# Kernel optimization log

Hardware: AMD Instinct MI355X
Metric: run time of the kernel (lower is better)

The kernel has to match this reference:

```python
import jax, jax.numpy as jnp
import numpy as np

FIXED_FRAMES = 30
# MediaPipe Holistic landmark layout: 468 face, 21 left hand, 33 pose, 21 right hand = 543
LIPS = np.array([61, 185, 40, 39, 37, 0, 267, 269, 270, 409, 291,
                 146, 91, 181, 84, 17, 314, 405, 321, 375,
                 78, 191, 80, 81, 82, 13, 312, 311, 310, 415,
                 95, 88, 178, 87, 14, 317, 402, 318, 324, 308], dtype=np.int32)
LEFT_HAND = np.arange(468, 489, dtype=np.int32)          # 21
UPPER_BODY = np.arange(489, 489 + 25, dtype=np.int32)    # 25 upper-body pose landmarks
RIGHT_HAND = np.arange(522, 543, dtype=np.int32)         # 21
SEL = np.concatenate([LIPS, LEFT_HAND, UPPER_BODY, RIGHT_HAND])  # 107 landmarks

N_FRAMES = 16384
N_LANDMARKS = 543

def setup_inputs() -> dict:
    key = jax.random.key(0)
    k1, k2 = jax.random.split(key)
    x = jax.random.normal(k1, (N_FRAMES, N_LANDMARKS, 3), dtype=jnp.float32)
    nan_mask = jax.random.uniform(k2, x.shape) < 0.1
    x = jnp.where(nan_mask, jnp.nan, x)
    return {"x_in": x}

def _normalize_gather(x_in):
    # Global nan-aware mean over ALL elements (scalar), as x[~isnan(x)].mean()
    mask = ~jnp.isnan(x_in)
    cnt = jnp.sum(mask).astype(x_in.dtype)
    xs = jnp.where(mask, x_in, 0.0)
    mean = jnp.sum(xs) / cnt
    xc = jnp.where(mask, x_in - mean, 0.0)
    # torch.std of the centered non-NaN values (unbiased, re-subtracts its own mean)
    m2 = jnp.sum(xc) / cnt
    var = jnp.sum(jnp.where(mask, (xc - m2) ** 2, 0.0)) / (cnt - 1.0)
    std = jnp.sqrt(var)
    y = jnp.where(mask, xc / std, 0.0)  # normalize; NaN positions -> 0 (x[isnan]=0)
    return y[:, SEL, :]                  # gather lips|lhand|pose|rhand -> [T, 107, 3]

def _resample(y, T):
    # F.interpolate over frame axis to FIXED_FRAMES (static Python branch on shape)
    if T < FIXED_FRAMES:
        # mode='linear', align_corners=False
        pos = (jnp.arange(FIXED_FRAMES, dtype=y.dtype) + 0.5) * (T / FIXED_FRAMES) - 0.5
        pos = jnp.clip(pos, 0.0, T - 1.0)
        i0 = jnp.floor(pos).astype(jnp.int32)
        i1 = jnp.minimum(i0 + 1, T - 1)
        w = (pos - i0.astype(y.dtype))[:, None, None]
        return (1.0 - w) * y[i0] + w * y[i1]
    else:
        # mode='nearest-exact'
        idx = jnp.floor((jnp.arange(FIXED_FRAMES, dtype=jnp.float32) + 0.5) * (T / FIXED_FRAMES))
        idx = jnp.clip(idx.astype(jnp.int32), 0, T - 1)
        return y[idx]

def reference(x_in):
    T = x_in.shape[0]
    y = _normalize_gather(x_in)   # [T, 107, 3]
    return _resample(y, T)        # [30, 107, 3]
```

## Files before the change

kernel.cpp:

```cpp
#include <hip/hip_runtime.h>

#define FIXED_FRAMES 30
#define N_LM 543
#define N_SEL 107
#define NBLK 2048
#define NTHR 256

typedef float f32x4 __attribute__((ext_vector_type(4)));

__constant__ int c_sel[N_SEL] = {
    61, 185, 40, 39, 37, 0, 267, 269, 270, 409, 291,
    146, 91, 181, 84, 17, 314, 405, 321, 375,
    78, 191, 80, 81, 82, 13, 312, 311, 310, 415,
    95, 88, 178, 87, 14, 317, 402, 318, 324, 308,
    468, 469, 470, 471, 472, 473, 474, 475, 476, 477, 478,
    479, 480, 481, 482, 483, 484, 485, 486, 487, 488,
    489, 490, 491, 492, 493, 494, 495, 496, 497, 498, 499,
    500, 501, 502, 503, 504, 505, 506, 507, 508, 509, 510,
    511, 512, 513,
    522, 523, 524, 525, 526, 527, 528, 529, 530, 531, 532,
    533, 534, 535, 536, 537, 538, 539, 540, 541, 542
};


__device__ __forceinline__ void acc4v(f32x4 v, f32x4& s, f32x4& s2, unsigned& c) {
    bool ok0 = (v.x == v.x), ok1 = (v.y == v.y), ok2 = (v.z == v.z), ok3 = (v.w == v.w);
    float z0 = ok0 ? v.x : 0.0f;
    float z1 = ok1 ? v.y : 0.0f;
    float z2 = ok2 ? v.z : 0.0f;
    float z3 = ok3 ? v.w : 0.0f;
    s.x += z0; s.y += z1; s.z += z2; s.w += z3;
    s2.x = fmaf(z0, z0, s2.x);
    s2.y = fmaf(z1, z1, s2.y);
    s2.z = fmaf(z2, z2, s2.z);
    s2.w = fmaf(z3, z3, s2.w);
    c += (unsigned)ok0 + (unsigned)ok1 + (unsigned)ok2 + (unsigned)ok3;
}

__device__ __forceinline__ f32x4 ntload(const f32x4* p) {
    return __builtin_nontemporal_load(p);
}

__global__ __launch_bounds__(NTHR) void fp_reduce(const f32x4* __restrict__ x, int n4,
                                                  double* __restrict__ ws) {
    f32x4 sA = {0, 0, 0, 0}, s2A = {0, 0, 0, 0};
    f32x4 sB = {0, 0, 0, 0}, s2B = {0, 0, 0, 0};
    unsigned int c = 0;

    int idx = blockIdx.x * NTHR + threadIdx.x;
    const int stride = NBLK * NTHR;

    int i = idx;
    if (i + 7 * stride < n4) {
        f32x4 v0 = ntload(&x[i]);
        f32x4 v1 = ntload(&x[i + stride]);
        f32x4 v2 = ntload(&x[i + 2 * stride]);
        f32x4 v3 = ntload(&x[i + 3 * stride]);
        f32x4 v4 = ntload(&x[i + 4 * stride]);
        f32x4 v5 = ntload(&x[i + 5 * stride]);
        f32x4 v6 = ntload(&x[i + 6 * stride]);
        f32x4 v7 = ntload(&x[i + 7 * stride]);
        acc4v(v0, sA, s2A, c); acc4v(v1, sB, s2B, c);
        acc4v(v2, sA, s2A, c); acc4v(v3, sB, s2B, c);
        acc4v(v4, sA, s2A, c); acc4v(v5, sB, s2B, c);
        acc4v(v6, sA, s2A, c); acc4v(v7, sB, s2B, c);
        i += 8 * stride;
    }
    if (i + 3 * stride < n4) {
        f32x4 v0 = ntload(&x[i]);
        f32x4 v1 = ntload(&x[i + stride]);
        f32x4 v2 = ntload(&x[i + 2 * stride]);
        f32x4 v3 = ntload(&x[i + 3 * stride]);
        acc4v(v0, sA, s2A, c); acc4v(v1, sB, s2B, c);
        acc4v(v2, sA, s2A, c); acc4v(v3, sB, s2B, c);
        i += 4 * stride;
    }
    for (; i < n4; i += stride) {
        acc4v(ntload(&x[i]), sA, s2A, c);
    }

    double sd = ((double)sA.x + (double)sA.y) + ((double)sA.z + (double)sA.w)
              + ((double)sB.x + (double)sB.y) + ((double)sB.z + (double)sB.w);
    double s2d = ((double)s2A.x + (double)s2A.y) + ((double)s2A.z + (double)s2A.w)
               + ((double)s2B.x + (double)s2B.y) + ((double)s2B.z + (double)s2B.w);
#pragma unroll
    for (int off = 32; off > 0; off >>= 1) {
        sd  += __shfl_down(sd, off, 64);
        s2d += __shfl_down(s2d, off, 64);
        c   += __shfl_down(c, off, 64);
    }

    __shared__ double ls[4], ls2[4];
    __shared__ unsigned int lc[4];
    int lane = threadIdx.x & 63;
    int wave = threadIdx.x >> 6;
    if (lane == 0) { ls[wave] = sd; ls2[wave] = s2d; lc[wave] = c; }
    __syncthreads();
    if (threadIdx.x == 0) {
        double bs = 0.0, bs2 = 0.0;
        unsigned long long bc = 0;
#pragma unroll
        for (int w = 0; w < 4; ++w) { bs += ls[w]; bs2 += ls2[w]; bc += lc[w]; }
        ws[blockIdx.x]            = bs;
        ws[NBLK + blockIdx.x]     = bs2;
        ws[2 * NBLK + blockIdx.x] = (double)bc;
    }
}

__global__ __launch_bounds__(NTHR) void fp_gather(const float* __restrict__ x,
                                                  const double* __restrict__ ws,
                                                  float* __restrict__ out, int T) {
    double s = 0.0, s2 = 0.0, c = 0.0;
    for (int i = threadIdx.x; i < NBLK; i += NTHR) {
        s  += ws[i];
        s2 += ws[NBLK + i];
        c  += ws[2 * NBLK + i];
    }
#pragma unroll
    for (int off = 32; off > 0; off >>= 1) {
        s  += __shfl_down(s, off, 64);
        s2 += __shfl_down(s2, off, 64);
        c  += __shfl_down(c, off, 64);
    }
    __shared__ double ls[4], ls2[4], lc[4];
    __shared__ double sm_mean, sm_inv_std;
    int lane = threadIdx.x & 63;
    int wave = threadIdx.x >> 6;
    if (lane == 0) { ls[wave] = s; ls2[wave] = s2; lc[wave] = c; }
    __syncthreads();
    if (threadIdx.x == 0) {
        double S1 = 0.0, S2 = 0.0, dc = 0.0;
#pragma unroll
        for (int w = 0; w < 4; ++w) { S1 += ls[w]; S2 += ls2[w]; dc += lc[w]; }

        double mean = S1 / dc;
        double m2 = (S1 - dc * mean) / dc;
        double mu = mean + m2;
        double var = (S2 - 2.0 * mu * S1 + dc * mu * mu) / (dc - 1.0);
        sm_mean = mean;
        sm_inv_std = 1.0 / sqrt(var);
    }
    __syncthreads();

    int t = blockIdx.x * NTHR + threadIdx.x;
    const int total = FIXED_FRAMES * N_SEL * 3;
    if (t >= total) return;

    double mean = sm_mean;
    double inv_std = sm_inv_std;

    int f = t / (N_SEL * 3);
    int r = t - f * (N_SEL * 3);
    int l = r / 3;
    int ch = r - l * 3;

    float scale = (float)T / 30.0f;
    int fi = (int)floorf(((float)f + 0.5f) * scale);
    if (fi > T - 1) fi = T - 1;
    if (fi < 0) fi = 0;

    float v = x[(size_t)fi * (N_LM * 3) + (size_t)c_sel[l] * 3 + ch];
    out[t] = (v == v) ? (float)(((double)v - mean) * inv_std) : 0.0f;
}

extern "C" void kernel_launch(void* const* d_in, const int* in_sizes, int n_in,
                              void* d_out, int out_size, void* d_ws, size_t ws_size,
                              hipStream_t stream) {
    const float* x = (const float*)d_in[0];
    float* out = (float*)d_out;
    double* ws = (double*)d_ws;

    int n = in_sizes[0];
    int n4 = n / 4;
    int T = n / (N_LM * 3);

    fp_reduce<<<NBLK, NTHR, 0, stream>>>((const f32x4*)x, n4, ws);

    const int total = FIXED_FRAMES * N_SEL * 3;
    fp_gather<<<(total + NTHR - 1) / NTHR, NTHR, 0, stream>>>(x, ws, out, T);
}
```

Baseline: 25.97 us.

## Fuse reduction and gather into one kernel with last-block ticket

Merges the global statistics reduction and the gather/normalize kernel into a single launch: every block writes its partials and takes an atomic ticket, and the last block to finish reduces all partials and writes the 30x107x3 output in a loop. A memset of the ticket is added before the launch. Nontemporal loads are replaced by plain loads, which may change cache behaviour. The goal is to cut the second kernel launch and the gap between kernels, but the final gather now runs serially on a single block and the memset adds its own operation.

```diff
diff --git a/kernel.cpp b/kernel.cpp
--- a/kernel.cpp
+++ b/kernel.cpp
@@ -37,12 +37,12 @@
     c += (unsigned)ok0 + (unsigned)ok1 + (unsigned)ok2 + (unsigned)ok3;
 }
 
-__device__ __forceinline__ f32x4 ntload(const f32x4* p) {
-    return __builtin_nontemporal_load(p);
-}
-
-__global__ __launch_bounds__(NTHR) void fp_reduce(const f32x4* __restrict__ x, int n4,
-                                                  double* __restrict__ ws) {
+__global__ __launch_bounds__(NTHR) void fp_fused(const f32x4* __restrict__ x4,
+                                                 const float* __restrict__ x,
+                                                 double* __restrict__ ws,
+                                                 unsigned* __restrict__ ticket,
+                                                 float* __restrict__ out,
+                                                 int n4, int T) {
     f32x4 sA = {0, 0, 0, 0}, s2A = {0, 0, 0, 0};
     f32x4 sB = {0, 0, 0, 0}, s2B = {0, 0, 0, 0};
     unsigned int c = 0;
@@ -52,14 +52,14 @@
 
     int i = idx;
     if (i + 7 * stride < n4) {
-        f32x4 v0 = ntload(&x[i]);
-        f32x4 v1 = ntload(&x[i + stride]);
-        f32x4 v2 = ntload(&x[i + 2 * stride]);
-        f32x4 v3 = ntload(&x[i + 3 * stride]);
-        f32x4 v4 = ntload(&x[i + 4 * stride]);
-        f32x4 v5 = ntload(&x[i + 5 * stride]);
-        f32x4 v6 = ntload(&x[i + 6 * stride]);
-        f32x4 v7 = ntload(&x[i + 7 * stride]);
+        f32x4 v0 = x4[i];
+        f32x4 v1 = x4[i + stride];
+        f32x4 v2 = x4[i + 2 * stride];
+        f32x4 v3 = x4[i + 3 * stride];
+        f32x4 v4 = x4[i + 4 * stride];
+        f32x4 v5 = x4[i + 5 * stride];
+        f32x4 v6 = x4[i + 6 * stride];
+        f32x4 v7 = x4[i + 7 * stride];
         acc4v(v0, sA, s2A, c); acc4v(v1, sB, s2B, c);
         acc4v(v2, sA, s2A, c); acc4v(v3, sB, s2B, c);
         acc4v(v4, sA, s2A, c); acc4v(v5, sB, s2B, c);
@@ -67,17 +67,15 @@
         i += 8 * stride;
     }
     if (i + 3 * stride < n4) {
-        f32x4 v0 = ntload(&x[i]);
-        f32x4 v1 = ntload(&x[i + stride]);
-        f32x4 v2 = ntload(&x[i + 2 * stride]);
-        f32x4 v3 = ntload(&x[i + 3 * stride]);
+        f32x4 v0 = x4[i];
+        f32x4 v1 = x4[i + stride];
+        f32x4 v2 = x4[i + 2 * stride];
+        f32x4 v3 = x4[i + 3 * stride];
         acc4v(v0, sA, s2A, c); acc4v(v1, sB, s2B, c);
         acc4v(v2, sA, s2A, c); acc4v(v3, sB, s2B, c);
         i += 4 * stride;
     }
-    for (; i < n4; i += stride) {
-        acc4v(ntload(&x[i]), sA, s2A, c);
-    }
+    for (; i < n4; i += stride) acc4v(x4[i], sA, s2A, c);
 
     double sd = ((double)sA.x + (double)sA.y) + ((double)sA.z + (double)sA.w)
               + ((double)sB.x + (double)sB.y) + ((double)sB.z + (double)sB.w);
@@ -92,6 +90,7 @@
 
     __shared__ double ls[4], ls2[4];
     __shared__ unsigned int lc[4];
+    __shared__ bool s_last;
     int lane = threadIdx.x & 63;
     int wave = threadIdx.x >> 6;
     if (lane == 0) { ls[wave] = sd; ls2[wave] = s2d; lc[wave] = c; }
@@ -104,34 +103,35 @@
         ws[blockIdx.x]            = bs;
         ws[NBLK + blockIdx.x]     = bs2;
         ws[2 * NBLK + blockIdx.x] = (double)bc;
+        __threadfence();
+        unsigned tk = atomicAdd(ticket, 1u);
+        s_last = (tk == NBLK - 1);
     }
-}
+    __syncthreads();
+    if (!s_last) return;
 
-__global__ __launch_bounds__(NTHR) void fp_gather(const float* __restrict__ x,
-                                                  const double* __restrict__ ws,
-                                                  float* __restrict__ out, int T) {
-    double s = 0.0, s2 = 0.0, c = 0.0;
-    for (int i = threadIdx.x; i < NBLK; i += NTHR) {
-        s  += ws[i];
-        s2 += ws[NBLK + i];
-        c  += ws[2 * NBLK + i];
+    __threadfence();
+
+    double s = 0.0, s2 = 0.0, cn = 0.0;
+    for (int j = threadIdx.x; j < NBLK; j += NTHR) {
+        s  += ws[j];
+        s2 += ws[NBLK + j];
+        cn += ws[2 * NBLK + j];
     }
 #pragma unroll
     for (int off = 32; off > 0; off >>= 1) {
         s  += __shfl_down(s, off, 64);
         s2 += __shfl_down(s2, off, 64);
-        c  += __shfl_down(c, off, 64);
+        cn += __shfl_down(cn, off, 64);
     }
-    __shared__ double ls[4], ls2[4], lc[4];
+    __shared__ double fs[4], fs2[4], fc[4];
     __shared__ double sm_mean, sm_inv_std;
-    int lane = threadIdx.x & 63;
-    int wave = threadIdx.x >> 6;
-    if (lane == 0) { ls[wave] = s; ls2[wave] = s2; lc[wave] = c; }
+    if (lane == 0) { fs[wave] = s; fs2[wave] = s2; fc[wave] = cn; }
     __syncthreads();
     if (threadIdx.x == 0) {
         double S1 = 0.0, S2 = 0.0, dc = 0.0;
 #pragma unroll
-        for (int w = 0; w < 4; ++w) { S1 += ls[w]; S2 += ls2[w]; dc += lc[w]; }
+        for (int w = 0; w < 4; ++w) { S1 += fs[w]; S2 += fs2[w]; dc += fc[w]; }
 
         double mean = S1 / dc;
         double m2 = (S1 - dc * mean) / dc;
@@ -142,25 +142,25 @@
     }
     __syncthreads();
 
-    int t = blockIdx.x * NTHR + threadIdx.x;
-    const int total = FIXED_FRAMES * N_SEL * 3;
-    if (t >= total) return;
-
     double mean = sm_mean;
     double inv_std = sm_inv_std;
+    float scale = (float)T / 30.0f;
+    const int total = FIXED_FRAMES * N_SEL * 3;
 
-    int f = t / (N_SEL * 3);
-    int r = t - f * (N_SEL * 3);
-    int l = r / 3;
-    int ch = r - l * 3;
+#pragma unroll 4
+    for (int t = threadIdx.x; t < total; t += NTHR) {
+        int f = t / (N_SEL * 3);
+        int r = t - f * (N_SEL * 3);
+        int l = r / 3;
+        int ch = r - l * 3;
 
-    float scale = (float)T / 30.0f;
-    int fi = (int)floorf(((float)f + 0.5f) * scale);
-    if (fi > T - 1) fi = T - 1;
-    if (fi < 0) fi = 0;
+        int fi = (int)floorf(((float)f + 0.5f) * scale);
+        if (fi > T - 1) fi = T - 1;
+        if (fi < 0) fi = 0;
 
-    float v = x[(size_t)fi * (N_LM * 3) + (size_t)c_sel[l] * 3 + ch];
-    out[t] = (v == v) ? (float)(((double)v - mean) * inv_std) : 0.0f;
+        float v = x[(size_t)fi * (N_LM * 3) + (size_t)c_sel[l] * 3 + ch];
+        out[t] = (v == v) ? (float)(((double)v - mean) * inv_std) : 0.0f;
+    }
 }
 
 extern "C" void kernel_launch(void* const* d_in, const int* in_sizes, int n_in,
@@ -169,13 +169,13 @@
     const float* x = (const float*)d_in[0];
     float* out = (float*)d_out;
     double* ws = (double*)d_ws;
+    unsigned* ticket = (unsigned*)((char*)d_ws + (size_t)3 * NBLK * 8);
 
     int n = in_sizes[0];
     int n4 = n / 4;
     int T = n / (N_LM * 3);
 
-    fp_reduce<<<NBLK, NTHR, 0, stream>>>((const f32x4*)x, n4, ws);
+    hipMemsetAsync(ticket, 0, sizeof(unsigned), stream);
 
-    const int total = FIXED_FRAMES * N_SEL * 3;
-    fp_gather<<<(total + NTHR - 1) / NTHR, NTHR, 0, stream>>>(x, ws, out, T);
+    fp_fused<<<NBLK, NTHR, 0, stream>>>((const f32x4*)x, x, ws, ticket, out, n4, T);
 }
```

Result: slower. 100.7 us (+287.9%).
